# Kernel tuning notes

Measured on AMD Instinct MI355X. Metric: run time of the kernel, lower is better.

## Reference

```python
import jax, jax.numpy as jnp
import numpy as np
import math

H = 14
W = 14
MU_MAX = math.sqrt((H / 2) ** 2 + (W / 2) ** 2)
EPS = 1e-6
LN_EPS = 1e-5


def _distance_sq():
    fy = np.fft.fftfreq(H) * H
    fx = np.fft.rfftfreq(W) * W
    d = fy[:, None] ** 2 + fx[None, :] ** 2  # (H, W//2+1)
    return jnp.asarray(d[None, None], dtype=jnp.float32)  # (1,1,H,W//2+1)


def setup_inputs() -> dict:
    key = jax.random.key(0)
    k0, k1, k2 = jax.random.split(key, 3)
    B, C, HID = 256, 768, 192  # hidden = max(768//4, 8)
    return {
        "x": jax.random.normal(k0, (B, 197, C), jnp.float32),
        "ln_gamma": jnp.ones((C,), jnp.float32),
        "ln_beta": jnp.zeros((C,), jnp.float32),
        "w1": jax.random.normal(k1, (C, HID), jnp.float32) * 0.02,
        "b1": jnp.zeros((HID,), jnp.float32),
        "w2": jax.random.normal(k2, (HID, 2), jnp.float32) * 0.02,
        "b2": jnp.zeros((2,), jnp.float32),
        "residual_scale": jnp.asarray(1e-4, jnp.float32),
    }


def reference(x, ln_gamma, ln_beta, w1, b1, w2, b2, residual_scale):
    b, _, c = x.shape
    cls_tok = x[:, :1]          # (B,1,C)
    xs = x[:, 1:]               # (B,196,C) raw spatial tokens
    # LayerNorm (biased variance, eps=1e-5 like torch default)
    mu_ln = xs.mean(-1, keepdims=True)
    var_ln = xs.var(-1, keepdims=True)
    xn = (xs - mu_ln) / jnp.sqrt(var_ln + LN_EPS) * ln_gamma + ln_beta
    # to (B,C,H,W) grid
    xg = xn.transpose(0, 2, 1).reshape(b, c, H, W)
    xm = xg.mean((-2, -1), keepdims=True)
    spec = jnp.fft.rfft2(xg - xm, norm='ortho')  # (B,C,H,W//2+1) complex
    energy = jnp.log1p(jnp.abs(spec)).mean((-2, -1))  # (B,C)
    hdn = jax.nn.gelu(energy @ w1 + b1, approximate=False)
    out2 = hdn @ w2 + b2  # (B,2)
    mu = jnp.maximum(MU_MAX * jax.nn.sigmoid(out2[:, 0]), 1.0).reshape(b, 1, 1, 1)
    sigma = jnp.maximum(jax.nn.softplus(out2[:, 1]), 0.1).reshape(b, 1, 1, 1)
    mask = jnp.exp(-_distance_sq() / (2.0 * mu ** 2 * sigma + EPS))
    filtered = jnp.fft.irfft2(spec * mask, s=(H, W), norm='ortho') + xm
    toks = filtered.reshape(b, c, H * W).transpose(0, 2, 1)  # (B,196,C)
    delta = toks - xn
    return jnp.concatenate([cls_tok, xs + residual_scale * delta], axis=1)
```

## Files before the change

kernel.cpp:

```cpp
#include <hip/hip_runtime.h>
#include <hip/hip_fp16.h>
#include <math.h>

#define NB    256
#define NTOKP 197
#define NTOK  196
#define NC    768
#define NHID  192
#define NH    14
#define NVF   8
#define CHT   64
#define NTILE 12
#define NCH   8
#define CCH   (NC / NCH)

constexpr float CT14[14] = {
    1.0f, 0.9009688679024191f, 0.6234898018587336f, 0.22252093395631445f,
    -0.22252093395631434f, -0.6234898018587335f, -0.9009688679024191f, -1.0f,
    -0.9009688679024191f, -0.6234898018587335f, -0.22252093395631434f,
    0.22252093395631445f, 0.6234898018587336f, 0.9009688679024191f};
constexpr float ST14[14] = {
    0.0f, 0.4338837391175581f, 0.7818314824680298f, 0.9749279121818236f,
    0.9749279121818236f, 0.7818314824680299f, 0.43388373911755823f, 0.0f,
    -0.43388373911755823f, -0.7818314824680299f, -0.9749279121818236f,
    -0.9749279121818236f, -0.7818314824680298f, -0.4338837391175581f};

__global__ __launch_bounds__(256) void k_stats(const float* __restrict__ x,
                                               float2* __restrict__ msv) {
  int row = blockIdx.x * 4 + (threadIdx.x >> 6);
  int lane = threadIdx.x & 63;
  if (row >= NB * NTOK) return;
  int b = row / NTOK, t = row - b * NTOK;
  const float4* p = (const float4*)(x + ((size_t)b * NTOKP + 1 + t) * NC);
  float s = 0.f, ss = 0.f;
#pragma unroll
  for (int k = 0; k < 3; ++k) {
    float4 v = p[lane + k * 64];
    s += v.x + v.y + v.z + v.w;
    ss += v.x * v.x + v.y * v.y + v.z * v.z + v.w * v.w;
  }
#pragma unroll
  for (int off = 32; off; off >>= 1) {
    s += __shfl_down(s, off);
    ss += __shfl_down(ss, off);
  }
  if (lane == 0) {
    float m = s * (1.f / NC);
    float var = ss * (1.f / NC) - m * m;
    msv[row] = make_float2(m, rsqrtf(var + 1e-5f));
  }
}

__global__ __launch_bounds__(256) void k_fwd(const float* __restrict__ x,
                                             const float* __restrict__ gamma,
                                             const float* __restrict__ beta,
                                             const float2* __restrict__ msv,
                                             float* __restrict__ energy) {
  __shared__ __half2 A[NH * NVF * CHT];
  __shared__ float2 ms[NTOK];
  __shared__ float esum[256];
  int b = blockIdx.y, c0 = blockIdx.x * CHT, tid = threadIdx.x;
  int c = tid & 63, w = tid >> 6;

  for (int k = tid; k < NTOK; k += 256) ms[k] = msv[b * NTOK + k];
  float g = gamma[c0 + c], be = beta[c0 + c];

  __half2 TW1[14], TW2[14];
#pragma unroll
  for (int k = 0; k < 14; ++k) {
    TW1[k] = __floats2half2_rn(CT14[k], -ST14[k]);
    TW2[k] = __floats2half2_rn(ST14[k], CT14[k]);
  }
  __syncthreads();

#pragma unroll 1
  for (int i = w; i < NH; i += 4) {
    const float* xr = x + ((size_t)b * NTOKP + 1 + i * NH) * NC + c0 + c;
    __half2 xh[NH];
#pragma unroll
    for (int j = 0; j < NH; ++j) {
      float2 m = ms[i * NH + j];
      xh[j] = __float2half2_rn((xr[(size_t)j * NC] - m.x) * m.y * g + be);
    }
    __half2 acc[NVF];
#pragma unroll
    for (int v = 0; v < NVF; ++v) acc[v] = __floats2half2_rn(0.f, 0.f);
#pragma unroll
    for (int j = 0; j < NH; ++j) {
#pragma unroll
      for (int v = 0; v < NVF; ++v)
        acc[v] = __hfma2(xh[j], TW1[(v * j) % 14], acc[v]);
    }
#pragma unroll
    for (int v = 0; v < NVF; ++v) A[(i * NVF + v) * CHT + c] = acc[v];
  }
  __syncthreads();

  float part = 0.f;
#pragma unroll 1
  for (int vv = 0; vv < 2; ++vv) {
    int v = w * 2 + vv;
    bool herm = (v == 0) || (v == 7);
    const __half2* Ac = A + v * CHT + c;
    __half2 E[7], O[7];
#pragma unroll
    for (int k = 0; k < 7; ++k) {
      E[k] = __floats2half2_rn(0.f, 0.f);
      O[k] = __floats2half2_rn(0.f, 0.f);
    }
#pragma unroll
    for (int m = 0; m < 7; ++m) {
      __half2 ae = Ac[(2 * m) * NVF * CHT];
      __half2 ao = Ac[(2 * m + 1) * NVF * CHT];
      __half2 aer = __low2half2(ae), aei = __high2half2(ae);
      __half2 aor = __low2half2(ao), aoi = __high2half2(ao);
#pragma unroll
      for (int k = 0; k < 7; ++k) {
        int t = (2 * k * m) % 14;
        E[k] = __hfma2(aer, TW1[t], __hfma2(aei, TW2[t], E[k]));
        O[k] = __hfma2(aor, TW1[t], __hfma2(aoi, TW2[t], O[k]));
      }
    }
    float pa = 1.f, pb = 1.f;
#pragma unroll
    for (int u = 0; u < 14; ++u) {
      if (!herm || u < 8) {
        int k = u % 7;
        __half2 Ov = O[k];
        __half2 S = __hfma2(__low2half2(Ov), TW1[u],
                            __hfma2(__high2half2(Ov), TW2[u], E[k]));
        float2 s2 = __half22float2(S);
        float mag = 14.f + __builtin_amdgcn_sqrtf(fmaf(s2.x, s2.x, s2.y * s2.y));
        if (herm) {
          float msq = mag * mag;
          if (u == 0) {
            if (v == 7) pb *= mag;
          } else if (u <= 3) {
            pa *= msq;
          } else if (u <= 6) {
            pb *= msq;
          } else {
            pb *= mag;
          }
        } else {
          if (u < 7) pa *= mag; else pb *= mag;
        }
      }
    }
    part += __logf(pa) + __logf(pb);
  }
  esum[tid] = part;
  __syncthreads();
  if (w == 0) {
    float e = esum[c] + esum[c + 64] + esum[c + 128] + esum[c + 192];
    energy[(size_t)b * NC + c0 + c] =
        (e - 111.f * 2.6390573296152584f) * (1.f / 112.f);
  }
}

__global__ __launch_bounds__(192) void k_mlp1(const float* __restrict__ energy,
                                              const float* __restrict__ w1,
                                              float* __restrict__ partial) {
  int s = blockIdx.x, b = blockIdx.y;
  int h = threadIdx.x;
  const float* ep = energy + (size_t)b * NC + s * CCH;
  const float* wp = w1 + (size_t)s * CCH * NHID + h;
  float acc = 0.f;
#pragma unroll 8
  for (int cc = 0; cc < CCH; ++cc)
    acc = fmaf(ep[cc], wp[(size_t)cc * NHID], acc);
  partial[((size_t)b * NCH + s) * NHID + h] = acc;
}

__global__ __launch_bounds__(192) void k_final(const float* __restrict__ partial,
                                               const float* __restrict__ b1,
                                               const float* __restrict__ w2,
                                               const float* __restrict__ b2,
                                               float* __restrict__ m2s) {
  __shared__ float2 sh[NHID];
  int b = blockIdx.x, h = threadIdx.x;
  float a = b1[h];
#pragma unroll
  for (int s = 0; s < NCH; ++s) a += partial[((size_t)b * NCH + s) * NHID + h];
  float ge = 0.5f * a * (1.f + erff(a * 0.70710678118654752f));
  sh[h] = make_float2(ge * w2[2 * h], ge * w2[2 * h + 1]);
  __syncthreads();
  if (h < 64) {
    float p0 = sh[h].x + sh[h + 64].x + sh[h + 128].x;
    float p1 = sh[h].y + sh[h + 64].y + sh[h + 128].y;
#pragma unroll
    for (int off = 32; off; off >>= 1) {
      p0 += __shfl_down(p0, off);
      p1 += __shfl_down(p1, off);
    }
    if (h == 0) {
      float o0 = p0 + b2[0], o1 = p1 + b2[1];
      float muv = 9.899494936611665f / (1.f + expf(-o0));
      muv = fmaxf(muv, 1.f);
      float sp = (o1 > 20.f) ? o1 : log1pf(expf(o1));
      float sg = fmaxf(sp, 0.1f);
      m2s[b] = 2.f * muv * muv * sg + 1e-6f;
    }
  }
}

__global__ __launch_bounds__(256) void k_inv(const float* __restrict__ x,
                                             const float* __restrict__ gamma,
                                             const float* __restrict__ beta,
                                             const float2* __restrict__ msv,
                                             const float* __restrict__ m2s,
                                             const float* __restrict__ rscale,
                                             float* __restrict__ out) {
  __shared__ __half2 T[NH * 7 * CHT];
  __shared__ float2 ms[NTOK];
  __shared__ float wexp[NH];
  __shared__ float kc[NH];
  int b = blockIdx.y, c0 = blockIdx.x * CHT, tid = threadIdx.x;
  int c = tid & 63, w = tid >> 6;
  float rs = rscale[0];

  for (int k = tid; k < NTOK; k += 256) ms[k] = msv[b * NTOK + k];
  if (tid < CHT) {
    size_t idx = (size_t)b * NTOKP * NC + c0 + tid;
    out[idx] = x[idx];
  }
  float msb = m2s[b];
  if (tid < NH) {
    int f = (tid <= 7) ? tid : 14 - tid;
    wexp[tid] = __expf(-(float)(f * f) / msb);
  }
  __syncthreads();
  if (tid < NH) {
    float s = 0.f;
#pragma unroll
    for (int k = 0; k < NH; ++k) s = fmaf(wexp[k], CT14[(k * tid) % 14], s);
    kc[tid] = s * (1.f / 14.f);
  }
  float g = gamma[c0 + c], be = beta[c0 + c];
  __syncthreads();

  float kr[NH];
#pragma unroll
  for (int d = 0; d < NH; ++d) kr[d] = kc[d];
  __half2 khp[NH];
#pragma unroll
  for (int d = 0; d < NH; ++d) khp[d] = __floats2half2_rn(kr[d], kr[(d + 1) % 14]);

#pragma unroll 1
  for (int i = w; i < NH; i += 4) {
    const float* xr = x + ((size_t)b * NTOKP + 1 + i * NH) * NC + c0 + c;
    __half2 xh[NH];
#pragma unroll
    for (int j = 0; j < NH; ++j) {
      float2 m = ms[i * NH + j];
      xh[j] = __float2half2_rn((xr[(size_t)j * NC] - m.x) * m.y * g + be);
    }
#pragma unroll
    for (int jp = 0; jp < 7; ++jp) {
      __half2 acc = __floats2half2_rn(0.f, 0.f);
#pragma unroll
      for (int j = 0; j < NH; ++j)
        acc = __hfma2(xh[j], khp[(2 * jp - j + 28) % 14], acc);
      T[(i * 7 + jp) * CHT + c] = acc;
    }
  }
  __syncthreads();

#pragma unroll 1
  for (int jq = w; jq < NH; jq += 4) {
    int jp = jq >> 1, hi = jq & 1;
    __half2 acc2[7];
#pragma unroll
    for (int d = 0; d < 7; ++d) acc2[d] = __floats2half2_rn(0.f, 0.f);
#pragma unroll
    for (int i = 0; i < NH; ++i) {
      __half2 t = T[(i * 7 + jp) * CHT + c];
      __half2 yi = hi ? __high2half2(t) : __low2half2(t);
#pragma unroll
      for (int d = 0; d < 7; ++d)
        acc2[d] = __hfma2(yi, khp[(2 * d - i + 28) % 14], acc2[d]);
    }
    const float* xr = x + ((size_t)b * NTOKP + 1 + jq) * NC + c0 + c;
    float* outr = out + ((size_t)b * NTOKP + 1 + jq) * NC + c0 + c;
#pragma unroll
    for (int ii = 0; ii < NH; ++ii) {
      float z = (ii & 1) ? __high2float(acc2[ii >> 1]) : __low2float(acc2[ii >> 1]);
      float xv = xr[(size_t)ii * NH * NC];
      float2 m = ms[ii * NH + jq];
      float xn = (xv - m.x) * m.y * g + be;
      outr[(size_t)ii * NH * NC] = xv + rs * (z - xn);
    }
  }
}

extern "C" void kernel_launch(void* const* d_in, const int* in_sizes, int n_in,
                              void* d_out, int out_size, void* d_ws, size_t ws_size,
                              hipStream_t stream) {
  (void)in_sizes; (void)n_in; (void)out_size; (void)ws_size;
  const float* x      = (const float*)d_in[0];
  const float* gamma  = (const float*)d_in[1];
  const float* beta   = (const float*)d_in[2];
  const float* w1     = (const float*)d_in[3];
  const float* b1     = (const float*)d_in[4];
  const float* w2     = (const float*)d_in[5];
  const float* b2     = (const float*)d_in[6];
  const float* rscale = (const float*)d_in[7];
  float* out = (float*)d_out;

  char* wsb = (char*)d_ws;
  float2* msv    = (float2*)(wsb + 0);
  float* energy  = (float*)(wsb + 401408);
  float* partial = (float*)(wsb + 1187840);
  float* m2s     = (float*)(wsb + 2760704);

  k_stats<<<(NB * NTOK + 3) / 4, 256, 0, stream>>>(x, msv);
  k_fwd<<<dim3(NTILE, NB), 256, 0, stream>>>(x, gamma, beta, msv, energy);
  k_mlp1<<<dim3(NCH, NB), 192, 0, stream>>>(energy, w1, partial);
  k_final<<<NB, 192, 0, stream>>>(partial, b1, w2, b2, m2s);
  k_inv<<<dim3(NTILE, NB), 256, 0, stream>>>(x, gamma, beta, msv, m2s, rscale,
                                             out);
}
```

Measured before the change: 144.4 us.

## Cache normalized activations as fp16 and reconstruct x in the inverse pass

The stats kernel now also writes a LayerNorm-normalized fp16 copy of the spatial tokens. The forward and inverse kernels read this half-precision copy instead of re-reading and re-normalizing fp32 x. The inverse kernel rebuilds x from the fp16 value through 1/gamma and 1/rstd, so it never re-reads fp32 x, which cuts global memory traffic. Scratch buffers for energy and partial sums move into the tail of the output buffer, which is overwritten later. The trade-off is fp16 rounding in the residual passthrough, a division by gamma that breaks if gamma is zero, and a dependence on workspace size.

After: 140.6 us. -2.6%, faster.

```diff
diff --git a/kernel.cpp b/kernel.cpp
--- a/kernel.cpp
+++ b/kernel.cpp
@@ -25,45 +25,74 @@
     -0.43388373911755823f, -0.7818314824680299f, -0.9749279121818236f,
     -0.9749279121818236f, -0.7818314824680298f, -0.4338837391175581f};
 
+__device__ __forceinline__ unsigned int h2bits(__half2 h) {
+  return *(unsigned int*)&h;
+}
+
+template <bool WH>
 __global__ __launch_bounds__(256) void k_stats(const float* __restrict__ x,
-                                               float2* __restrict__ msv) {
+                                               const float* __restrict__ gamma,
+                                               const float* __restrict__ beta,
+                                               float2* __restrict__ msv,
+                                               __half* __restrict__ xnh) {
   int row = blockIdx.x * 4 + (threadIdx.x >> 6);
   int lane = threadIdx.x & 63;
   if (row >= NB * NTOK) return;
   int b = row / NTOK, t = row - b * NTOK;
   const float4* p = (const float4*)(x + ((size_t)b * NTOKP + 1 + t) * NC);
+  float4 v[3];
   float s = 0.f, ss = 0.f;
 #pragma unroll
   for (int k = 0; k < 3; ++k) {
-    float4 v = p[lane + k * 64];
-    s += v.x + v.y + v.z + v.w;
-    ss += v.x * v.x + v.y * v.y + v.z * v.z + v.w * v.w;
-  }
-#pragma unroll
-  for (int off = 32; off; off >>= 1) {
-    s += __shfl_down(s, off);
-    ss += __shfl_down(ss, off);
-  }
-  if (lane == 0) {
-    float m = s * (1.f / NC);
-    float var = ss * (1.f / NC) - m * m;
-    msv[row] = make_float2(m, rsqrtf(var + 1e-5f));
-  }
-}
-
+    v[k] = p[lane + k * 64];
+    s += v[k].x + v[k].y + v[k].z + v[k].w;
+    ss += v[k].x * v[k].x + v[k].y * v[k].y + v[k].z * v[k].z + v[k].w * v[k].w;
+  }
+#pragma unroll
+  for (int m = 32; m; m >>= 1) {
+    s += __shfl_xor(s, m);
+    ss += __shfl_xor(ss, m);
+  }
+  float mean = s * (1.f / NC);
+  float var = ss * (1.f / NC) - mean * mean;
+  float rstd = rsqrtf(var + 1e-5f);
+  if (lane == 0) msv[row] = make_float2(mean, rstd);
+  if (WH) {
+#pragma unroll
+    for (int k = 0; k < 3; ++k) {
+      float4 g = ((const float4*)gamma)[lane + k * 64];
+      float4 be = ((const float4*)beta)[lane + k * 64];
+      float4 xn;
+      xn.x = (v[k].x - mean) * rstd * g.x + be.x;
+      xn.y = (v[k].y - mean) * rstd * g.y + be.y;
+      xn.z = (v[k].z - mean) * rstd * g.z + be.z;
+      xn.w = (v[k].w - mean) * rstd * g.w + be.w;
+      uint2 u = make_uint2(h2bits(__floats2half2_rn(xn.x, xn.y)),
+                           h2bits(__floats2half2_rn(xn.z, xn.w)));
+      *(uint2*)(xnh + (size_t)row * NC + lane * 4 + k * 256) = u;
+    }
+  }
+}
+
+template <bool UH>
 __global__ __launch_bounds__(256) void k_fwd(const float* __restrict__ x,
+                                             const __half* __restrict__ xnh,
                                              const float* __restrict__ gamma,
                                              const float* __restrict__ beta,
                                              const float2* __restrict__ msv,
                                              float* __restrict__ energy) {
   __shared__ __half2 A[NH * NVF * CHT];
-  __shared__ float2 ms[NTOK];
+  __shared__ float2 ms[UH ? 1 : NTOK];
   __shared__ float esum[256];
   int b = blockIdx.y, c0 = blockIdx.x * CHT, tid = threadIdx.x;
   int c = tid & 63, w = tid >> 6;
 
-  for (int k = tid; k < NTOK; k += 256) ms[k] = msv[b * NTOK + k];
-  float g = gamma[c0 + c], be = beta[c0 + c];
+  float g = 0.f, be = 0.f;
+  if (!UH) {
+    for (int k = tid; k < NTOK; k += 256) ms[k] = msv[b * NTOK + k];
+    g = gamma[c0 + c];
+    be = beta[c0 + c];
+  }
 
   __half2 TW1[14], TW2[14];
 #pragma unroll
@@ -75,12 +104,18 @@
 
 #pragma unroll 1
   for (int i = w; i < NH; i += 4) {
-    const float* xr = x + ((size_t)b * NTOKP + 1 + i * NH) * NC + c0 + c;
     __half2 xh[NH];
-#pragma unroll
-    for (int j = 0; j < NH; ++j) {
-      float2 m = ms[i * NH + j];
-      xh[j] = __float2half2_rn((xr[(size_t)j * NC] - m.x) * m.y * g + be);
+    if (UH) {
+      const __half* xr = xnh + ((size_t)b * NTOK + i * NH) * NC + c0 + c;
+#pragma unroll
+      for (int j = 0; j < NH; ++j) xh[j] = __half2half2(xr[(size_t)j * NC]);
+    } else {
+      const float* xr = x + ((size_t)b * NTOKP + 1 + i * NH) * NC + c0 + c;
+#pragma unroll
+      for (int j = 0; j < NH; ++j) {
+        float2 m = ms[i * NH + j];
+        xh[j] = __float2half2_rn((xr[(size_t)j * NC] - m.x) * m.y * g + be);
+      }
     }
     __half2 acc[NVF];
 #pragma unroll
@@ -204,7 +239,9 @@
   }
 }
 
+template <bool UH>
 __global__ __launch_bounds__(256) void k_inv(const float* __restrict__ x,
+                                             const __half* __restrict__ xnh,
                                              const float* __restrict__ gamma,
                                              const float* __restrict__ beta,
                                              const float2* __restrict__ msv,
@@ -213,13 +250,18 @@
                                              float* __restrict__ out) {
   __shared__ __half2 T[NH * 7 * CHT];
   __shared__ float2 ms[NTOK];
+  __shared__ float rr[UH ? NTOK : 1];
   __shared__ float wexp[NH];
   __shared__ float kc[NH];
   int b = blockIdx.y, c0 = blockIdx.x * CHT, tid = threadIdx.x;
   int c = tid & 63, w = tid >> 6;
   float rs = rscale[0];
 
-  for (int k = tid; k < NTOK; k += 256) ms[k] = msv[b * NTOK + k];
+  for (int k = tid; k < NTOK; k += 256) {
+    float2 m = msv[b * NTOK + k];
+    ms[k] = m;
+    if (UH) rr[k] = 1.f / m.y;
+  }
   if (tid < CHT) {
     size_t idx = (size_t)b * NTOKP * NC + c0 + tid;
     out[idx] = x[idx];
@@ -237,6 +279,7 @@
     kc[tid] = s * (1.f / 14.f);
   }
   float g = gamma[c0 + c], be = beta[c0 + c];
+  float rg = 1.f / g;
   __syncthreads();
 
   float kr[NH];
@@ -248,12 +291,18 @@
 
 #pragma unroll 1
   for (int i = w; i < NH; i += 4) {
-    const float* xr = x + ((size_t)b * NTOKP + 1 + i * NH) * NC + c0 + c;
     __half2 xh[NH];
-#pragma unroll
-    for (int j = 0; j < NH; ++j) {
-      float2 m = ms[i * NH + j];
-      xh[j] = __float2half2_rn((xr[(size_t)j * NC] - m.x) * m.y * g + be);
+    if (UH) {
+      const __half* xr = xnh + ((size_t)b * NTOK + i * NH) * NC + c0 + c;
+#pragma unroll
+      for (int j = 0; j < NH; ++j) xh[j] = __half2half2(xr[(size_t)j * NC]);
+    } else {
+      const float* xr = x + ((size_t)b * NTOKP + 1 + i * NH) * NC + c0 + c;
+#pragma unroll
+      for (int j = 0; j < NH; ++j) {
+        float2 m = ms[i * NH + j];
+        xh[j] = __float2half2_rn((xr[(size_t)j * NC] - m.x) * m.y * g + be);
+      }
     }
 #pragma unroll
     for (int jp = 0; jp < 7; ++jp) {
@@ -280,15 +329,23 @@
       for (int d = 0; d < 7; ++d)
         acc2[d] = __hfma2(yi, khp[(2 * d - i + 28) % 14], acc2[d]);
     }
+    float* outr = out + ((size_t)b * NTOKP + 1 + jq) * NC + c0 + c;
+    const __half* xq = xnh + ((size_t)b * NTOK + jq) * NC + c0 + c;
     const float* xr = x + ((size_t)b * NTOKP + 1 + jq) * NC + c0 + c;
-    float* outr = out + ((size_t)b * NTOKP + 1 + jq) * NC + c0 + c;
 #pragma unroll
     for (int ii = 0; ii < NH; ++ii) {
       float z = (ii & 1) ? __high2float(acc2[ii >> 1]) : __low2float(acc2[ii >> 1]);
-      float xv = xr[(size_t)ii * NH * NC];
-      float2 m = ms[ii * NH + jq];
-      float xn = (xv - m.x) * m.y * g + be;
-      outr[(size_t)ii * NH * NC] = xv + rs * (z - xn);
+      if (UH) {
+        float xnv = __half2float(xq[(size_t)ii * NH * NC]);
+        int t = ii * NH + jq;
+        float xv = fmaf((xnv - be) * rg, rr[t], ms[t].x);
+        outr[(size_t)ii * NH * NC] = xv + rs * (z - xnv);
+      } else {
+        float xv = xr[(size_t)ii * NH * NC];
+        float2 m = ms[ii * NH + jq];
+        float xn = (xv - m.x) * m.y * g + be;
+        outr[(size_t)ii * NH * NC] = xv + rs * (z - xn);
+      }
     }
   }
 }
@@ -296,7 +353,7 @@
 extern "C" void kernel_launch(void* const* d_in, const int* in_sizes, int n_in,
                               void* d_out, int out_size, void* d_ws, size_t ws_size,
                               hipStream_t stream) {
-  (void)in_sizes; (void)n_in; (void)out_size; (void)ws_size;
+  (void)in_sizes; (void)n_in; (void)out_size;
   const float* x      = (const float*)d_in[0];
   const float* gamma  = (const float*)d_in[1];
   const float* beta   = (const float*)d_in[2];
@@ -308,15 +365,31 @@
   float* out = (float*)d_out;
 
   char* wsb = (char*)d_ws;
-  float2* msv    = (float2*)(wsb + 0);
-  float* energy  = (float*)(wsb + 401408);
-  float* partial = (float*)(wsb + 1187840);
-  float* m2s     = (float*)(wsb + 2760704);
-
-  k_stats<<<(NB * NTOK + 3) / 4, 256, 0, stream>>>(x, msv);
-  k_fwd<<<dim3(NTILE, NB), 256, 0, stream>>>(x, gamma, beta, msv, energy);
+  float2* msv = (float2*)(wsb + 0);
+  float* m2s  = (float*)(wsb + 401408);
+  __half* xnh = (__half*)(wsb + 402432);
+  size_t need = 402432 + (size_t)NB * NTOK * NC * 2;
+  bool useH = ws_size >= need;
+
+  float* energy  = (float*)((char*)d_out + 150994944);
+  float* partial = (float*)((char*)d_out + 152043520);
+
+  if (useH) {
+    k_stats<true><<<NB * NTOK / 4, 256, 0, stream>>>(x, gamma, beta, msv, xnh);
+    k_fwd<true><<<dim3(NTILE, NB), 256, 0, stream>>>(x, xnh, gamma, beta, msv,
+                                                     energy);
+  } else {
+    k_stats<false><<<NB * NTOK / 4, 256, 0, stream>>>(x, gamma, beta, msv, xnh);
+    k_fwd<false><<<dim3(NTILE, NB), 256, 0, stream>>>(x, xnh, gamma, beta, msv,
+                                                      energy);
+  }
   k_mlp1<<<dim3(NCH, NB), 192, 0, stream>>>(energy, w1, partial);
   k_final<<<NB, 192, 0, stream>>>(partial, b1, w2, b2, m2s);
-  k_inv<<<dim3(NTILE, NB), 256, 0, stream>>>(x, gamma, beta, msv, m2s, rscale,
-                                             out);
-}
+  if (useH) {
+    k_inv<true><<<dim3(NTILE, NB), 256, 0, stream>>>(x, xnh, gamma, beta, msv,
+                                                     m2s, rscale, out);
+  } else {
+    k_inv<false><<<dim3(NTILE, NB), 256, 0, stream>>>(x, xnh, gamma, beta, msv,
+                                                      m2s, rscale, out);
+  }
+}
```
